# Kernel optimization log

Measured on AMD Instinct MI355X. Metric: run time of the kernel, lower is better.

The kernel has to match this reference:

```python
import jax, jax.numpy as jnp
import numpy as np

N_POINTS = 16384
D_MODEL = 512
K = 16
N_RES_BLOCKS = 4


def _linear_params(key, d_in, d_out):
    kw, kb = jax.random.split(key)
    bound = 1.0 / np.sqrt(d_in)
    w = jax.random.uniform(kw, (d_out, d_in), jnp.float32, -bound, bound)
    b = jax.random.uniform(kb, (d_out,), jnp.float32, -bound, bound)
    return w, b


def setup_inputs() -> dict:
    key = jax.random.key(0)
    ks = jax.random.split(key, 7)
    inputs = jax.random.normal(ks[0], (N_POINTS, 3), jnp.float32)
    knn = jax.random.randint(ks[1], (N_POINTS, K), 0, N_POINTS, jnp.int64)
    d4, d2 = D_MODEL // 4, D_MODEL // 2
    w_mlp1, b_mlp1 = _linear_params(ks[2], D_MODEL, d4)
    w_lfa1, b_lfa1 = _linear_params(ks[3], 4, d4)
    w_lfa2, b_lfa2 = _linear_params(ks[4], 4, d2)
    w_mlp2, b_mlp2 = _linear_params(ks[5], D_MODEL, D_MODEL)
    w_res, b_res = _linear_params(ks[6], D_MODEL, D_MODEL)
    return {
        "inputs": inputs, "knn": knn,
        "w_mlp1": w_mlp1, "b_mlp1": b_mlp1,
        "w_lfa1": w_lfa1, "b_lfa1": b_lfa1,
        "w_lfa2": w_lfa2, "b_lfa2": b_lfa2,
        "w_mlp2": w_mlp2, "b_mlp2": b_mlp2,
        "w_res": w_res, "b_res": b_res,
    }


def _lfa(feats, geo, knn, w, b):
    # feats: [N, d_in], geo: [N, K, 4] -> [N, 2*d_in]
    g = geo @ w.T + b                      # [N, K, d_in]
    nbr = feats[knn]                       # [N, K, d_in] gather
    return jnp.concatenate([g, nbr], axis=2).mean(axis=1)


def reference(inputs, knn, w_mlp1, b_mlp1, w_lfa1, b_lfa1,
              w_lfa2, b_lfa2, w_mlp2, b_mlp2, w_res, b_res):
    # geometric features: diff to each neighbor + its norm -> [N, K, 4]
    diff = inputs[:, None, :] - inputs[knn]
    norm = jnp.linalg.norm(diff, axis=-1, keepdims=True)
    geo = jnp.concatenate([diff, norm], axis=-1)

    f0 = jnp.zeros((N_POINTS, D_MODEL), jnp.float32)
    for _ in range(N_RES_BLOCKS):  # weights are shared across blocks
        x = f0 @ w_mlp1.T + b_mlp1                 # [N, d/4]
        x = _lfa(x, geo, knn, w_lfa1, b_lfa1)      # [N, d/2]
        x = _lfa(x, geo, knn, w_lfa2, b_lfa2)      # [N, d]
        x = x @ w_mlp2.T + b_mlp2 + f0             # ResBlock residual
        x = x + (f0 @ w_res.T + b_res)             # outer residual mlp
        f0 = x
    return f0
```

## Files before the change

### kernel.cpp

```cpp
#include <hip/hip_runtime.h>
#include <math.h>

#define NPTS 16384
#define KNB  16
#define D    512


__device__ __forceinline__ void onehop8(int t, const int* __restrict__ knn,
                                        const float4* __restrict__ in,
                                        float4* __restrict__ out) {
  int n = t >> 3, k = t & 7;
  float4 g1 = in[knn[n * KNB + k]];
  float4 g2 = in[knn[n * KNB + k + 8]];
  float ax = g1.x + g2.x, ay = g1.y + g2.y;
  float az = g1.z + g2.z, aw = g1.w + g2.w;
#pragma unroll
  for (int o = 1; o < 8; o <<= 1) {
    ax += __shfl_xor(ax, o, 64); ay += __shfl_xor(ay, o, 64);
    az += __shfl_xor(az, o, 64); aw += __shfl_xor(aw, o, 64);
  }
  if (k == 0) {
    const float r = 1.f / 16.f;
    out[n] = make_float4(ax * r, ay * r, az * r, aw * r);
  }
}

__device__ __forceinline__ float4 red16(float ax, float ay, float az,
                                        float aw) {
#pragma unroll
  for (int o = 1; o < 16; o <<= 1) {
    ax += __shfl_xor(ax, o, 64); ay += __shfl_xor(ay, o, 64);
    az += __shfl_xor(az, o, 64); aw += __shfl_xor(aw, o, 64);
  }
  return make_float4(ax, ay, az, aw);
}

__device__ __forceinline__ void fstep66(
    int fb, int tid, int first, const float* __restrict__ Fprev,
    const float* __restrict__ zbuf, const float* __restrict__ Rm,
    const float* __restrict__ Mt, float* __restrict__ Fnext) {
  __shared__ float sA[512], sB[512];
  __shared__ double redm[16][256];
  const int r = fb >> 1, jbase = (fb & 1) * 256;
  const int rm = (r >= 8 && r < 32) ? (r - 8) : (r == 32 ? 32 : -1);
  if (tid < 512) {
    sA[tid] = first
        ? ((r < 8) ? zbuf[r * D + tid] : (r == 32 ? zbuf[8 * D + tid] : 0.f))
        : Fprev[r * D + tid];
  } else {
    int kk = tid - 512;
    float v = 0.f;
    if (rm >= 0)
      v = first ? ((rm < 8) ? zbuf[rm * D + kk]
                            : (rm == 32 ? zbuf[8 * D + kk] : 0.f))
                : Fprev[rm * D + kk];
    sB[kk] = v;
  }
  __syncthreads();
  const int q = tid & 63, kc = tid >> 6;
  const int j0 = jbase + q * 4, k0 = kc * 32;
  double a0 = 0, a1 = 0, a2 = 0, a3 = 0;
#pragma unroll 2
  for (int k = 0; k < 32; ++k) {
    const float4 rv = *(const float4*)(Rm + (size_t)(k0 + k) * D + j0);
    const float4 mv = *(const float4*)(Mt + (size_t)(k0 + k) * D + j0);
    const double a = (double)sA[k0 + k], b = (double)sB[k0 + k];
    a0 += a * (double)rv.x + b * (double)mv.x;
    a1 += a * (double)rv.y + b * (double)mv.y;
    a2 += a * (double)rv.z + b * (double)mv.z;
    a3 += a * (double)rv.w + b * (double)mv.w;
  }
  redm[kc][q * 4 + 0] = a0; redm[kc][q * 4 + 1] = a1;
  redm[kc][q * 4 + 2] = a2; redm[kc][q * 4 + 3] = a3;
  __syncthreads();
  if (tid < 256) {
    double s = 0.0;
#pragma unroll
    for (int u = 0; u < 16; ++u) s += redm[u][tid];
    int j = jbase + tid;
    float cb = (r < 8) ? zbuf[r * D + j] : (r == 32 ? zbuf[8 * D + j] : 0.f);
    Fnext[r * D + j] = (float)(s + (double)cb);
  }
}

__global__ __launch_bounds__(256) void prep_kernel(
    const float* __restrict__ pts, const int* __restrict__ raw,
    const float* __restrict__ w_mlp1, const float* __restrict__ b_mlp1,
    const float* __restrict__ w_lfa1, const float* __restrict__ b_lfa1,
    const float* __restrict__ w_lfa2, const float* __restrict__ b_lfa2,
    const float* __restrict__ w_mlp2, const float* __restrict__ b_mlp2,
    const float* __restrict__ w_res, const float* __restrict__ b_res,
    int* __restrict__ knn_i, float4* __restrict__ sbase,
    float* __restrict__ zbuf, float* __restrict__ Mt,
    float* __restrict__ Rm) {
  const bool is64 = (raw[1] == 0) && (raw[3] == 0) && (raw[5] == 0) &&
                    (raw[7] == 0);
  const int t = blockIdx.x * 256 + threadIdx.x;
  knn_i[t] = is64 ? raw[2 * t] : raw[t];
  {
    int n = t >> 4, k = t & 15;
    int idx = is64 ? raw[2 * (n * KNB + k)] : raw[n * KNB + k];
    float dx = pts[n * 3 + 0] - pts[idx * 3 + 0];
    float dy = pts[n * 3 + 1] - pts[idx * 3 + 1];
    float dz = pts[n * 3 + 2] - pts[idx * 3 + 2];
    float nr = sqrtf(dx * dx + dy * dy + dz * dz);
    float4 s = red16(dx, dy, dz, nr);
    if (k == 0) {
      const float r = 1.f / 16.f;
      sbase[n] = make_float4(s.x * r, s.y * r, s.z * r, s.w * r);
    }
  }
  if (t < 32768) {
    int j = t >> 6, lane = t & 63;
    const float* wrow = w_mlp2 + (size_t)j * D;
    double acc[9];
#pragma unroll
    for (int u = 0; u < 9; ++u) acc[u] = 0.0;
#pragma unroll
    for (int it = 0; it < 8; ++it) {
      int i = lane + 64 * it;
      double w = wrow[i];
      if (i < 256) {
        acc[0] += w * w_lfa2[i * 4 + 0]; acc[1] += w * w_lfa2[i * 4 + 1];
        acc[2] += w * w_lfa2[i * 4 + 2]; acc[3] += w * w_lfa2[i * 4 + 3];
        acc[8] += w * b_lfa2[i];
      } else if (i < 384) {
        int q = i - 256;
        acc[4] += w * w_lfa1[q * 4 + 0]; acc[5] += w * w_lfa1[q * 4 + 1];
        acc[6] += w * w_lfa1[q * 4 + 2]; acc[7] += w * w_lfa1[q * 4 + 3];
        acc[8] += w * b_lfa1[q];
      } else {
        acc[8] += w * b_mlp1[i - 384];
      }
    }
#pragma unroll
    for (int u = 0; u < 9; ++u) {
      double v = acc[u];
#pragma unroll
      for (int o = 32; o > 0; o >>= 1) v += __shfl_down(v, o, 64);
      if (lane == 0) {
        if (u == 8) v += (double)b_mlp2[j] + (double)b_res[j];
        zbuf[u * D + j] = (float)v;
      }
    }
  }
  {
    int a = t & 511, b = t >> 9;
    const float* wrow = w_mlp2 + (size_t)b * D + 384;
    double s0 = 0.0, s1 = 0.0, s2 = 0.0, s3 = 0.0;
#pragma unroll 8
    for (int i = 0; i < 128; i += 4) {
      s0 += (double)wrow[i + 0] * (double)w_mlp1[(size_t)(i + 0) * D + a];
      s1 += (double)wrow[i + 1] * (double)w_mlp1[(size_t)(i + 1) * D + a];
      s2 += (double)wrow[i + 2] * (double)w_mlp1[(size_t)(i + 2) * D + a];
      s3 += (double)wrow[i + 3] * (double)w_mlp1[(size_t)(i + 3) * D + a];
    }
    Mt[(size_t)a * D + b] = (float)((s0 + s1) + (s2 + s3));
  }
  {
    int i = t & 511, j = t >> 9;
    Rm[(size_t)i * D + j] = w_res[(size_t)j * D + i] + ((i == j) ? 1.0f : 0.0f);
  }
}

__global__ __launch_bounds__(1024) void hop_kernel(
    const int* __restrict__ knn, const float4* __restrict__ sin,
    float4* __restrict__ sout, const float* __restrict__ zbuf,
    const float* __restrict__ Rm, const float* __restrict__ Mt,
    const float* __restrict__ Fprev, float* __restrict__ Fnext, int first) {
  const int tid = threadIdx.x;
  if (blockIdx.x < 128) {
    onehop8(blockIdx.x * 1024 + tid, knn, sin, sout);
  } else {
    fstep66((int)blockIdx.x - 128, tid, first, Fprev, zbuf, Rm, Mt, Fnext);
  }
}

__global__ __launch_bounds__(1024, 4) void out_kernel(
    const int* __restrict__ knn, const float4* __restrict__ sbase,
    const float* __restrict__ Ecat, float* __restrict__ outp) {
  const int tid = threadIdx.x;
  const int n0 = blockIdx.x * 64;
  __shared__ float4 s_t[8][64];
  {
    int pt = tid >> 4, k = tid & 15;
    float4 g = sbase[(size_t)6 * NPTS + knn[(n0 + pt) * KNB + k]];
    float4 s = red16(g.x, g.y, g.z, g.w);
    if (k == 0) {
      const float r = 1.f / 16.f;
      s_t[7][pt] = make_float4(s.x * r, s.y * r, s.z * r, s.w * r);
    }
  }
  if (tid < 448) {
    int k = tid / 64, pt = tid & 63;
    s_t[k][pt] = sbase[(size_t)k * NPTS + n0 + pt];
  }
  __syncthreads();
  const int col2 = tid & 255;
  const int ptg = tid >> 8;
  float2 tab[33];
#pragma unroll
  for (int r = 0; r < 33; ++r)
    tab[r] = *(const float2*)(Ecat + r * D + col2 * 2);
#pragma unroll
  for (int it = 0; it < 16; ++it) {
    int pt = ptg * 16 + it;
    float2 acc = tab[32];
#pragma unroll
    for (int k = 0; k < 8; ++k) {
      float4 s = s_t[k][pt];
      float2 e0 = tab[4 * k + 0], e1 = tab[4 * k + 1];
      float2 e2 = tab[4 * k + 2], e3 = tab[4 * k + 3];
      acc.x += s.x * e0.x + s.y * e1.x + s.z * e2.x + s.w * e3.x;
      acc.y += s.x * e0.y + s.y * e1.y + s.z * e2.y + s.w * e3.y;
    }
    *(float2*)(outp + (size_t)(n0 + pt) * D + col2 * 2) = acc;
  }
}

extern "C" void kernel_launch(void* const* d_in, const int* in_sizes, int n_in,
                              void* d_out, int out_size, void* d_ws,
                              size_t ws_size, hipStream_t stream) {
  const float* inputs = (const float*)d_in[0];
  const int* knn_raw  = (const int*)d_in[1];
  const float* w_mlp1 = (const float*)d_in[2];
  const float* b_mlp1 = (const float*)d_in[3];
  const float* w_lfa1 = (const float*)d_in[4];
  const float* b_lfa1 = (const float*)d_in[5];
  const float* w_lfa2 = (const float*)d_in[6];
  const float* b_lfa2 = (const float*)d_in[7];
  const float* w_mlp2 = (const float*)d_in[8];
  const float* b_mlp2 = (const float*)d_in[9];
  const float* w_res  = (const float*)d_in[10];
  const float* b_res  = (const float*)d_in[11];
  float* out = (float*)d_out;

  float*  ws    = (float*)d_ws;
  float4* sbase = (float4*)(ws + 0);
  float*  zbuf  = ws + 524288;
  float*  F2    = ws + 528896;
  float*  F3    = ws + 545792;
  float*  Ecat  = ws + 562688;
  int*    knn_i = (int*)(ws + 579584);
  float*  Mt    = ws + 841728;
  float*  Rm    = ws + 1103872;

  prep_kernel<<<1024, 256, 0, stream>>>(inputs, knn_raw, w_mlp1, b_mlp1,
                                        w_lfa1, b_lfa1, w_lfa2, b_lfa2,
                                        w_mlp2, b_mlp2, w_res, b_res,
                                        knn_i, sbase, zbuf, Mt, Rm);
  float4* s0 = (float4*)sbase;
  hop_kernel<<<194, 1024, 0, stream>>>(knn_i, s0, s0 + NPTS, zbuf, Rm, Mt,
                                       (const float*)nullptr, F2, 1);
  hop_kernel<<<128, 1024, 0, stream>>>(knn_i, s0 + NPTS, s0 + 2 * NPTS, zbuf,
                                       Rm, Mt, (const float*)nullptr,
                                       (float*)nullptr, 0);
  hop_kernel<<<194, 1024, 0, stream>>>(knn_i, s0 + 2 * NPTS, s0 + 3 * NPTS,
                                       zbuf, Rm, Mt, F2, F3, 0);
  hop_kernel<<<128, 1024, 0, stream>>>(knn_i, s0 + 3 * NPTS, s0 + 4 * NPTS,
                                       zbuf, Rm, Mt, (const float*)nullptr,
                                       (float*)nullptr, 0);
  hop_kernel<<<194, 1024, 0, stream>>>(knn_i, s0 + 4 * NPTS, s0 + 5 * NPTS,
                                       zbuf, Rm, Mt, F3, Ecat, 0);
  hop_kernel<<<128, 1024, 0, stream>>>(knn_i, s0 + 5 * NPTS, s0 + 6 * NPTS,
                                       zbuf, Rm, Mt, (const float*)nullptr,
                                       (float*)nullptr, 0);
  out_kernel<<<256, 1024, 0, stream>>>(knn_i, sbase, Ecat, out);
}
```

Before: 159.7 us.

## Compute two-hop neighbor averages directly to halve hop kernel launches

Adds a twohop4 routine that averages over neighbors-of-neighbors (256 gathers per point) straight from an earlier level, so two hop levels can be produced in the same launch. The chain of seven hop launches shrinks to three, and the one-hop gather is rebalanced to 4 threads per point. This trades fewer kernel boundaries and syncs for about 16x more random gathers per two-hop level, which increases memory traffic and latency per thread.

Result: slower. 267.0 us (+67.2%).

```diff
diff --git a/kernel.cpp b/kernel.cpp
--- a/kernel.cpp
+++ b/kernel.cpp
@@ -6,21 +6,55 @@
 #define D    512
 
 
-__device__ __forceinline__ void onehop8(int t, const int* __restrict__ knn,
+__device__ __forceinline__ void onehop4(int t, const int* __restrict__ knn,
                                         const float4* __restrict__ in,
                                         float4* __restrict__ out) {
-  int n = t >> 3, k = t & 7;
-  float4 g1 = in[knn[n * KNB + k]];
-  float4 g2 = in[knn[n * KNB + k + 8]];
-  float ax = g1.x + g2.x, ay = g1.y + g2.y;
-  float az = g1.z + g2.z, aw = g1.w + g2.w;
-#pragma unroll
-  for (int o = 1; o < 8; o <<= 1) {
+  int n = t >> 2, k = t & 3;
+  float4 g1 = in[knn[n * KNB + k + 0]];
+  float4 g2 = in[knn[n * KNB + k + 4]];
+  float4 g3 = in[knn[n * KNB + k + 8]];
+  float4 g4 = in[knn[n * KNB + k + 12]];
+  float ax = (g1.x + g2.x) + (g3.x + g4.x);
+  float ay = (g1.y + g2.y) + (g3.y + g4.y);
+  float az = (g1.z + g2.z) + (g3.z + g4.z);
+  float aw = (g1.w + g2.w) + (g3.w + g4.w);
+#pragma unroll
+  for (int o = 1; o < 4; o <<= 1) {
     ax += __shfl_xor(ax, o, 64); ay += __shfl_xor(ay, o, 64);
     az += __shfl_xor(az, o, 64); aw += __shfl_xor(aw, o, 64);
   }
   if (k == 0) {
     const float r = 1.f / 16.f;
+    out[n] = make_float4(ax * r, ay * r, az * r, aw * r);
+  }
+}
+
+__device__ __forceinline__ void twohop4(int t, const int* __restrict__ knn,
+                                        const float4* __restrict__ in,
+                                        float4* __restrict__ out) {
+  int n = t >> 2, k = t & 3;
+  float ax = 0.f, ay = 0.f, az = 0.f, aw = 0.f;
+#pragma unroll
+  for (int h = 0; h < 4; ++h) {
+    int a = knn[n * KNB + k + 4 * h];
+    const int4* rr = (const int4*)(knn + (size_t)a * KNB);
+#pragma unroll
+    for (int q = 0; q < 4; ++q) {
+      int4 i4 = rr[q];
+      float4 g;
+      g = in[i4.x]; ax += g.x; ay += g.y; az += g.z; aw += g.w;
+      g = in[i4.y]; ax += g.x; ay += g.y; az += g.z; aw += g.w;
+      g = in[i4.z]; ax += g.x; ay += g.y; az += g.z; aw += g.w;
+      g = in[i4.w]; ax += g.x; ay += g.y; az += g.z; aw += g.w;
+    }
+  }
+#pragma unroll
+  for (int o = 1; o < 4; o <<= 1) {
+    ax += __shfl_xor(ax, o, 64); ay += __shfl_xor(ay, o, 64);
+    az += __shfl_xor(az, o, 64); aw += __shfl_xor(aw, o, 64);
+  }
+  if (k == 0) {
+    const float r = 1.f / 256.f;
     out[n] = make_float4(ax * r, ay * r, az * r, aw * r);
   }
 }
@@ -164,13 +198,19 @@
 }
 
 __global__ __launch_bounds__(1024) void hop_kernel(
-    const int* __restrict__ knn, const float4* __restrict__ sin,
-    float4* __restrict__ sout, const float* __restrict__ zbuf,
+    const int* __restrict__ knn, const float4* __restrict__ sa_in,
+    float4* __restrict__ sa_out, int a_two, const float4* __restrict__ sb_in,
+    float4* __restrict__ sb_out, const float* __restrict__ zbuf,
     const float* __restrict__ Rm, const float* __restrict__ Mt,
     const float* __restrict__ Fprev, float* __restrict__ Fnext, int first) {
   const int tid = threadIdx.x;
-  if (blockIdx.x < 128) {
-    onehop8(blockIdx.x * 1024 + tid, knn, sin, sout);
+  if (blockIdx.x < 64) {
+    int t = blockIdx.x * 1024 + tid;
+    if (a_two) twohop4(t, knn, sa_in, sa_out);
+    else       onehop4(t, knn, sa_in, sa_out);
+  } else if (blockIdx.x < 128) {
+    int t = ((int)blockIdx.x - 64) * 1024 + tid;
+    twohop4(t, knn, sb_in, sb_out);
   } else {
     fstep66((int)blockIdx.x - 128, tid, first, Fprev, zbuf, Rm, Mt, Fnext);
   }
@@ -250,20 +290,14 @@
                                         w_mlp2, b_mlp2, w_res, b_res,
                                         knn_i, sbase, zbuf, Mt, Rm);
   float4* s0 = (float4*)sbase;
-  hop_kernel<<<194, 1024, 0, stream>>>(knn_i, s0, s0 + NPTS, zbuf, Rm, Mt,
+  hop_kernel<<<194, 1024, 0, stream>>>(knn_i, s0, s0 + NPTS, 0,
+                                       s0, s0 + 2 * NPTS, zbuf, Rm, Mt,
                                        (const float*)nullptr, F2, 1);
-  hop_kernel<<<128, 1024, 0, stream>>>(knn_i, s0 + NPTS, s0 + 2 * NPTS, zbuf,
-                                       Rm, Mt, (const float*)nullptr,
-                                       (float*)nullptr, 0);
-  hop_kernel<<<194, 1024, 0, stream>>>(knn_i, s0 + 2 * NPTS, s0 + 3 * NPTS,
-                                       zbuf, Rm, Mt, F2, F3, 0);
-  hop_kernel<<<128, 1024, 0, stream>>>(knn_i, s0 + 3 * NPTS, s0 + 4 * NPTS,
-                                       zbuf, Rm, Mt, (const float*)nullptr,
-                                       (float*)nullptr, 0);
-  hop_kernel<<<194, 1024, 0, stream>>>(knn_i, s0 + 4 * NPTS, s0 + 5 * NPTS,
-                                       zbuf, Rm, Mt, F3, Ecat, 0);
-  hop_kernel<<<128, 1024, 0, stream>>>(knn_i, s0 + 5 * NPTS, s0 + 6 * NPTS,
-                                       zbuf, Rm, Mt, (const float*)nullptr,
-                                       (float*)nullptr, 0);
+  hop_kernel<<<194, 1024, 0, stream>>>(knn_i, s0 + NPTS, s0 + 3 * NPTS, 1,
+                                       s0 + 2 * NPTS, s0 + 4 * NPTS, zbuf, Rm,
+                                       Mt, F2, F3, 0);
+  hop_kernel<<<194, 1024, 0, stream>>>(knn_i, s0 + 3 * NPTS, s0 + 5 * NPTS, 1,
+                                       s0 + 4 * NPTS, s0 + 6 * NPTS, zbuf, Rm,
+                                       Mt, F3, Ecat, 0);
   out_kernel<<<256, 1024, 0, stream>>>(knn_i, sbase, Ecat, out);
 }
```
